# Performance work log

Hardware: AMD Instinct MI355X
Metric: run time of the kernel (lower is better)

The kernel has to match this reference:

```python
import jax, jax.numpy as jnp
import numpy as np

D_MODEL = 1024
D_STATE = 16
D_CONV = 4
EXPAND = 1
D_INNER = EXPAND * D_MODEL  # must equal D_MODEL for original dt_proj shapes to work
BATCH = 2
SEQ = 2048


def silu(x):
    return x * jax.nn.sigmoid(x)


def setup_inputs() -> dict:
    key = jax.random.key(0)
    ks = jax.random.split(key, 8)
    s = 0.02
    return {
        "x": jax.random.normal(ks[0], (BATCH, SEQ, D_MODEL), dtype=jnp.float32),
        "W_in": jax.random.normal(ks[1], (2 * D_INNER, D_MODEL), dtype=jnp.float32) * s,
        "conv_w": jax.random.normal(ks[2], (D_INNER, D_CONV), dtype=jnp.float32) * s,
        "conv_b": jnp.zeros((D_INNER,), dtype=jnp.float32),
        "W_dt": jax.random.normal(ks[3], (D_INNER, D_INNER), dtype=jnp.float32) * s,
        "b_dt": jnp.zeros((D_INNER,), dtype=jnp.float32),
        "A_log": jnp.zeros((D_INNER, D_STATE), dtype=jnp.float32),  # torch: log(ones)=0
        "Bp": jax.random.normal(ks[4], (D_INNER, D_STATE), dtype=jnp.float32),
        "Cp": jax.random.normal(ks[5], (D_INNER, D_STATE), dtype=jnp.float32),
        "Dp": jnp.ones((D_INNER,), dtype=jnp.float32),
        "W_out": jax.random.normal(ks[6], (D_MODEL, D_INNER), dtype=jnp.float32) * s,
    }


def reference(x, W_in, conv_w, conv_b, W_dt, b_dt, A_log, Bp, Cp, Dp, W_out):
    B, L, _ = x.shape
    # in_proj then split into ssm branch and gating residual
    xr = x @ W_in.T                               # (B, L, 2*D_INNER)
    x_proj, res = jnp.split(xr, 2, axis=-1)       # each (B, L, D_INNER)

    # causal depthwise conv1d (kernel D_CONV), == torch conv1d(padding=K-1)[..., :L]
    xp = jnp.pad(x_proj, ((0, 0), (D_CONV - 1, 0), (0, 0)))
    xc = conv_b + sum(conv_w[:, k] * xp[:, k:k + L, :] for k in range(D_CONV))
    xc = silu(xc)                                 # (B, L, D_INNER)

    # selective SSM scan
    delta = jax.nn.softplus(xc @ W_dt.T + b_dt)   # (B, L, D_INNER)
    A = -jnp.exp(A_log)                           # (D_INNER, D_STATE)
    dA = jnp.exp(delta[..., None] * A)            # (B, L, D_INNER, D_STATE)
    dBx = delta[..., None] * Bp * xc[..., None]   # (B, L, D_INNER, D_STATE)

    def step(h, inp):
        dA_t, dBx_t = inp                         # (B, D_INNER, D_STATE)
        h = dA_t * h + dBx_t
        y = jnp.einsum('bdn,dn->bd', h, Cp)
        return h, y

    h0 = jnp.zeros((B, D_INNER, D_STATE), dtype=x.dtype)
    _, ys = jax.lax.scan(step, h0, (dA.transpose(1, 0, 2, 3), dBx.transpose(1, 0, 2, 3)))
    x_ssm = ys.transpose(1, 0, 2) + xc * Dp       # (B, L, D_INNER)

    return (x_ssm * silu(res)) @ W_out.T          # (B, L, D_MODEL)
```

## Files before the change

### kernel.cpp

```cpp
#include <hip/hip_runtime.h>

typedef unsigned short u16;
typedef __bf16 bf16;
typedef bf16 bf16x8 __attribute__((ext_vector_type(8)));
typedef float f32x4 __attribute__((ext_vector_type(4)));

#define SEQ     2048
#define BATCH   2
#define DM      1024
#define DI      1024
#define NROW    (BATCH*SEQ)
#define NSTATE  16
#define NCHUNK  64
#define CLEN    32

static_assert(SEQ == NCHUNK * CLEN, "chunking must cover SEQ");

__device__ __forceinline__ u16 f2bf(float f) {
  unsigned u = __builtin_bit_cast(unsigned, f);
  u += 0x7FFFu + ((u >> 16) & 1u);
  return (u16)(u >> 16);
}
__device__ __forceinline__ float bf2f(u16 u) {
  return __builtin_bit_cast(float, (unsigned)u << 16);
}
__device__ __forceinline__ float sigm(float x) { return 1.f / (1.f + __expf(-x)); }

__global__ __launch_bounds__(256) void k_cvt_all(
    const float* __restrict__ x, const float* __restrict__ Win,
    const float* __restrict__ Wdt, const float* __restrict__ Wout,
    u16* __restrict__ xbf, u16* __restrict__ winbf,
    u16* __restrict__ wdtbf, u16* __restrict__ woutbf)
{
  long i = (long)blockIdx.x * 256 + threadIdx.x;
  const float* src; u16* dst; long off;
  if (i < 1048576)            { src = x;    dst = xbf;    off = i; }
  else if (i < 1572864)       { src = Win;  dst = winbf;  off = i - 1048576; }
  else if (i < 1835008)       { src = Wdt;  dst = wdtbf;  off = i - 1572864; }
  else                        { src = Wout; dst = woutbf; off = i - 1835008; }
  float4 v = reinterpret_cast<const float4*>(src)[off];
  ushort4 o;
  o.x = f2bf(v.x); o.y = f2bf(v.y); o.z = f2bf(v.z); o.w = f2bf(v.w);
  reinterpret_cast<ushort4*>(dst)[off] = o;
}


__device__ __forceinline__ void gload16(const u16* g, u16* l) {
  __builtin_amdgcn_global_load_lds((const __attribute__((address_space(1))) void*)g,
                                   (__attribute__((address_space(3))) void*)l,
                                   16, 0, 0);
}

template<int EPI, int GX>
__global__ __launch_bounds__(256, 2) void k_gemm(
    const u16* __restrict__ A, const u16* __restrict__ B,
    float* __restrict__ outf, u16* __restrict__ outb, u16* __restrict__ outb2,
    const float* __restrict__ bias,
    const float* __restrict__ A_log, const float* __restrict__ Bp,
    float* __restrict__ hfin, float* __restrict__ sumdt,
    int M, int N, int K)
{
  __shared__ __align__(16) u16 smem[4 * 128 * 64];
  u16* sA = smem;
  u16* sB = smem + 2 * 128 * 64;
  const int t = threadIdx.x;
  const int wave = t >> 6, lane = t & 63;
  const int lr = lane & 15, kb = lane >> 4;
  const int wr = wave >> 1, wc = wave & 1;

  const int nwg = gridDim.x, bid = blockIdx.x;
  const int wg  = (bid & 7) * (nwg >> 3) + (bid >> 3);
  const long bm = (long)(wg / GX) * 128;
  const long bn = (long)(wg % GX) * 128;

  f32x4 acc[4][4] = {};

  const int srow = t >> 3;
  const int gslot8 = (((t & 7) ^ (srow & 7)) * 8);
  const u16* gA0 = A + (bm + srow) * (long)K + gslot8;
  const u16* gB0 = B + (bn + srow) * (long)K + gslot8;

  auto STAGE = [&](int buf, int k0) {
    #pragma unroll
    for (int i = 0; i < 4; ++i)
      gload16(gA0 + (long)i * 32 * K + k0, &sA[buf * 8192 + i * 2048 + wave * 512]);
    #pragma unroll
    for (int i = 0; i < 4; ++i)
      gload16(gB0 + (long)i * 32 * K + k0, &sB[buf * 8192 + i * 2048 + wave * 512]);
  };

  const int xr = lr & 7;
  STAGE(0, 0);
  __syncthreads();
  int cur = 0;
  for (int k0 = 0; k0 < K; k0 += 64) {
    if (k0 + 64 < K) STAGE(cur ^ 1, k0 + 64);
    const u16* pa = &sA[cur * 8192];
    const u16* pb = &sB[cur * 8192];
    bf16x8 af[2][4], bfr[2][4];
    #pragma unroll
    for (int ks = 0; ks < 2; ++ks) {
      const int co = ((ks * 4 + kb) ^ xr) * 8;
      #pragma unroll
      for (int mi = 0; mi < 4; ++mi)
        af[ks][mi] = *reinterpret_cast<const bf16x8*>(
            pa + (wr * 64 + mi * 16 + lr) * 64 + co);
      #pragma unroll
      for (int ni = 0; ni < 4; ++ni)
        bfr[ks][ni] = *reinterpret_cast<const bf16x8*>(
            pb + (wc * 64 + ni * 16 + lr) * 64 + co);
    }
    __builtin_amdgcn_s_setprio(1);
    #pragma unroll
    for (int ks = 0; ks < 2; ++ks)
      #pragma unroll
      for (int mi = 0; mi < 4; ++mi)
        #pragma unroll
        for (int ni = 0; ni < 4; ++ni)
          acc[mi][ni] = __builtin_amdgcn_mfma_f32_16x16x32_bf16(
              af[ks][mi], bfr[ks][ni], acc[mi][ni], 0, 0, 0);
    __builtin_amdgcn_s_setprio(0);
    __syncthreads();
    cur ^= 1;
  }

  float* sDelta = (float*)smem;

  #pragma unroll
  for (int mi = 0; mi < 4; ++mi) {
    const long row0 = bm + wr * 64 + mi * 16 + kb * 4;
    #pragma unroll
    for (int ni = 0; ni < 4; ++ni) {
      const long col = bn + wc * 64 + ni * 16 + lr;
      #pragma unroll
      for (int j = 0; j < 4; ++j) {
        const float v = acc[mi][ni][j];
        const long r = row0 + j;
        if (EPI == 0) {
          outf[r * N + col] = v;
        } else if (EPI == 1) {
          if (bn < DI) outb[r * DI + col] = f2bf(v);
          else         outb2[r * DI + (col - DI)] = f2bf(v * sigm(v));
        } else if (EPI == 3) {
          float z = v + bias[col];
          float sp = fmaxf(z, 0.f) + log1pf(__expf(-fabsf(z)));
          outb[r * N + col] = f2bf(sp);
          sDelta[(int)(r - bm) * 128 + (int)(col - bn)] = sp;
        }
      }
    }
  }

  if (EPI == 3) {
    __syncthreads();
    const int dl = t & 127;
    const int d  = (int)bn + dl;
    const int b  = (int)(bm >> 11);
    const int c0 = (int)((bm & 2047) >> 5);
    float Aa[NSTATE], Bb[NSTATE];
    #pragma unroll
    for (int n = 0; n < NSTATE; ++n) {
      Aa[n] = -__expf(A_log[d * NSTATE + n]);
      Bb[n] = Bp[d * NSTATE + n];
    }
    for (int cl = (t >> 7) * 2; cl < (t >> 7) * 2 + 2; ++cl) {
      float h[NSTATE];
      #pragma unroll
      for (int n = 0; n < NSTATE; ++n) h[n] = 0.f;
      float sdt = 0.f;
      const long grow0 = bm + cl * 32;
      for (int i = 0; i < CLEN; ++i) {
        float dt = sDelta[(cl * 32 + i) * 128 + dl];
        float xv = bf2f(A[(grow0 + i) * (long)K + d]);
        sdt += dt;
        float dx = dt * xv;
        #pragma unroll
        for (int n = 0; n < NSTATE; ++n) {
          float da = __expf(dt * Aa[n]);
          h[n] = fmaf(da, h[n], dx * Bb[n]);
        }
      }
      const int cg = c0 + cl;
      const long hb = ((long)(b * NCHUNK + cg) * NSTATE) * DI + d;
      #pragma unroll
      for (int n = 0; n < NSTATE; ++n) hfin[hb + (long)n * DI] = h[n];
      sumdt[(long)(b * NCHUNK + cg) * DI + d] = sdt;
    }
  }
}

__global__ __launch_bounds__(256) void k_conv(
    const u16* __restrict__ xproj, const float* __restrict__ convw,
    const float* __restrict__ convb, u16* __restrict__ xcbf)
{
  const int idx = blockIdx.x * 256 + threadIdx.x;
  const int d0 = (idx & 127) * 8;
  const int m  = idx >> 7;
  const int l  = m & (SEQ - 1);
  float acc[8];
  #pragma unroll
  for (int di = 0; di < 8; ++di) acc[di] = convb[d0 + di];
  #pragma unroll
  for (int k = 0; k < 4; ++k) {
    if (l + k - 3 >= 0) {
      ushort4 v2 = *reinterpret_cast<const ushort4*>(&xproj[(long)(m + k - 3) * DI + d0]);
      ushort4 v3 = *reinterpret_cast<const ushort4*>(&xproj[(long)(m + k - 3) * DI + d0 + 4]);
      const u16 vv[8] = {v2.x, v2.y, v2.z, v2.w, v3.x, v3.y, v3.z, v3.w};
      #pragma unroll
      for (int di = 0; di < 8; ++di)
        acc[di] = fmaf(convw[(d0 + di) * 4 + k], bf2f(vv[di]), acc[di]);
    }
  }
  u16 ov[8];
  #pragma unroll
  for (int di = 0; di < 8; ++di) {
    float s = acc[di] * sigm(acc[di]);
    ov[di] = f2bf(s);
  }
  ushort4 o0 = {ov[0], ov[1], ov[2], ov[3]}, o1 = {ov[4], ov[5], ov[6], ov[7]};
  *reinterpret_cast<ushort4*>(&xcbf[(long)m * DI + d0]) = o0;
  *reinterpret_cast<ushort4*>(&xcbf[(long)m * DI + d0 + 4]) = o1;
}

__global__ __launch_bounds__(256) void k_combine(
    const float* __restrict__ hfin, const float* __restrict__ sumdt_buf,
    const float* __restrict__ A_log, float* __restrict__ hstart)
{
  const int idx = blockIdx.x * 256 + threadIdx.x;
  const int d = idx & (DI - 1);
  const int n = (idx >> 10) & (NSTATE - 1);
  const int b = idx >> 14;
  const float Aa = -__expf(A_log[d * NSTATE + n]);
  float h = 0.f;
  for (int c = 0; c < NCHUNK; ++c) {
    const long sb = ((long)(b * NCHUNK + c) * NSTATE + n) * DI + d;
    hstart[sb] = h;
    float sdt = sumdt_buf[(long)(b * NCHUNK + c) * DI + d];
    h = fmaf(__expf(Aa * sdt), h, hfin[sb]);
  }
}

__global__ __launch_bounds__(256) void k_scanB(
    const u16* __restrict__ delta, const u16* __restrict__ xc,
    const float* __restrict__ A_log, const float* __restrict__ Bp,
    const float* __restrict__ Cp, const float* __restrict__ Dp,
    const u16* __restrict__ sres, const float* __restrict__ hstart,
    u16* __restrict__ gated)
{
  const int tid = threadIdx.x, blk = blockIdx.x;
  const int d = (blk & 3) * 256 + tid;
  const int c = (blk >> 2) & (NCHUNK - 1);
  const int b = blk >> 8;
  float Aa[NSTATE], Bb[NSTATE], Cc[NSTATE], h[NSTATE];
  #pragma unroll
  for (int n = 0; n < NSTATE; ++n) {
    Aa[n] = -__expf(A_log[d * NSTATE + n]);
    Bb[n] = Bp[d * NSTATE + n];
    Cc[n] = Cp[d * NSTATE + n];
  }
  const float Dd = Dp[d];
  const long sb = ((long)(b * NCHUNK + c) * NSTATE) * DI + d;
  #pragma unroll
  for (int n = 0; n < NSTATE; ++n) h[n] = hstart[sb + (long)n * DI];
  const long base = ((long)(b * SEQ + c * CLEN)) * DI + d;
  for (int i = 0; i < CLEN; ++i) {
    float dt = bf2f(delta[base + (long)i * DI]);
    float x  = bf2f(xc[base + (long)i * DI]);
    float dx = dt * x;
    float y = 0.f;
    #pragma unroll
    for (int n = 0; n < NSTATE; ++n) {
      float da = __expf(dt * Aa[n]);
      h[n] = fmaf(da, h[n], dx * Bb[n]);
      y = fmaf(h[n], Cc[n], y);
    }
    float xs = fmaf(x, Dd, y);
    float g = xs * bf2f(sres[base + (long)i * DI]);
    gated[base + (long)i * DI] = f2bf(g);
  }
}

extern "C" void kernel_launch(void* const* d_in, const int* in_sizes, int n_in,
                              void* d_out, int out_size, void* d_ws, size_t ws_size,
                              hipStream_t stream)
{
  const float* x      = (const float*)d_in[0];
  const float* W_in   = (const float*)d_in[1];
  const float* conv_w = (const float*)d_in[2];
  const float* conv_b = (const float*)d_in[3];
  const float* W_dt   = (const float*)d_in[4];
  const float* b_dt   = (const float*)d_in[5];
  const float* A_log  = (const float*)d_in[6];
  const float* Bp     = (const float*)d_in[7];
  const float* Cp     = (const float*)d_in[8];
  const float* Dp     = (const float*)d_in[9];
  const float* W_out  = (const float*)d_in[10];
  float* out = (float*)d_out;

  const long MD = (long)NROW * DI;

  char* ws = (char*)d_ws;
  u16*   xproj_bf = (u16*)ws;               ws += MD * 2;
  u16*   silu_bf  = (u16*)ws;               ws += MD * 2;
  u16*   delta_bf = (u16*)ws;               ws += MD * 2;
  u16*   xc_bf    = (u16*)ws;               ws += MD * 2;
  u16*   xbf      = (u16*)ws;               ws += MD * 2;
  u16*   Win_bf   = (u16*)ws;               ws += (long)2 * DI * DM * 2;
  u16*   Wdt_bf   = (u16*)ws;               ws += (long)DI * DI * 2;
  u16*   Wout_bf  = (u16*)ws;               ws += (long)DM * DI * 2;
  float* hfin     = (float*)ws;             ws += (long)BATCH * NCHUNK * NSTATE * DI * 4;
  float* sumdt    = (float*)ws;             ws += (long)BATCH * NCHUNK * DI * 4;
  float* hstart   = (float*)ws;             ws += (long)BATCH * NCHUNK * NSTATE * DI * 4;

  u16* gated = xbf;

  k_cvt_all<<<dim3(8192), dim3(256), 0, stream>>>(
      x, W_in, W_dt, W_out, xbf, Win_bf, Wdt_bf, Wout_bf);

  k_gemm<1, 16><<<dim3(512), dim3(256), 0, stream>>>(
      xbf, Win_bf, nullptr, xproj_bf, silu_bf, nullptr,
      nullptr, nullptr, nullptr, nullptr, NROW, 2 * DI, DM);

  k_conv<<<dim3((unsigned)(MD / 8 / 256)), dim3(256), 0, stream>>>(
      xproj_bf, conv_w, conv_b, xc_bf);

  k_gemm<3, 8><<<dim3(256), dim3(256), 0, stream>>>(
      xc_bf, Wdt_bf, nullptr, delta_bf, nullptr, b_dt,
      A_log, Bp, hfin, sumdt, NROW, DI, DI);

  k_combine<<<dim3(BATCH * NSTATE * DI / 256), dim3(256), 0, stream>>>(
      hfin, sumdt, A_log, hstart);
  k_scanB<<<dim3(BATCH * NCHUNK * (DI / 256)), dim3(256), 0, stream>>>(
      delta_bf, xc_bf, A_log, Bp, Cp, Dp, silu_bf, hstart, gated);

  k_gemm<0, 8><<<dim3(256), dim3(256), 0, stream>>>(
      gated, Wout_bf, out, nullptr, nullptr, nullptr,
      nullptr, nullptr, nullptr, nullptr, NROW, DM, DI);
}
```

Measured before the change: 169.5 us.

## Switch GEMM main loop to a 4-stage LDS ring with K-tile 32

```diff
diff --git a/kernel.cpp b/kernel.cpp
--- a/kernel.cpp
+++ b/kernel.cpp
@@ -60,9 +60,9 @@
     float* __restrict__ hfin, float* __restrict__ sumdt,
     int M, int N, int K)
 {
-  __shared__ __align__(16) u16 smem[4 * 128 * 64];
+  __shared__ __align__(16) u16 smem[32768];
   u16* sA = smem;
-  u16* sB = smem + 2 * 128 * 64;
+  u16* sB = smem + 16384;
   const int t = threadIdx.x;
   const int wave = t >> 6, lane = t & 63;
   const int lr = lane & 15, kb = lane >> 4;
@@ -75,54 +75,44 @@
 
   f32x4 acc[4][4] = {};
 
-  const int srow = t >> 3;
-  const int gslot8 = (((t & 7) ^ (srow & 7)) * 8);
+  const int srow = t >> 2;
+  const int gslot8 = (((t & 3) ^ (srow & 3)) * 8);
   const u16* gA0 = A + (bm + srow) * (long)K + gslot8;
   const u16* gB0 = B + (bn + srow) * (long)K + gslot8;
 
   auto STAGE = [&](int buf, int k0) {
-    #pragma unroll
-    for (int i = 0; i < 4; ++i)
-      gload16(gA0 + (long)i * 32 * K + k0, &sA[buf * 8192 + i * 2048 + wave * 512]);
-    #pragma unroll
-    for (int i = 0; i < 4; ++i)
-      gload16(gB0 + (long)i * 32 * K + k0, &sB[buf * 8192 + i * 2048 + wave * 512]);
+    gload16(gA0 + k0,            &sA[buf * 4096 + wave * 512]);
+    gload16(gA0 + 64 * (long)K + k0, &sA[buf * 4096 + 2048 + wave * 512]);
+    gload16(gB0 + k0,            &sB[buf * 4096 + wave * 512]);
+    gload16(gB0 + 64 * (long)K + k0, &sB[buf * 4096 + 2048 + wave * 512]);
   };
 
-  const int xr = lr & 7;
+  const int xr = lr & 3;
+  const int NT = K / 32;
   STAGE(0, 0);
+  STAGE(1, 32);
+  for (int tt = 0; tt < NT; ++tt) {
+    STAGE((tt + 2) & 3, (tt + 2 < NT) ? (tt + 2) * 32 : 0);
+    asm volatile("s_waitcnt vmcnt(8)\n\ts_barrier" ::: "memory");
+    const int cur = tt & 3;
+    const u16* pa = &sA[cur * 4096];
+    const u16* pb = &sB[cur * 4096];
+    const int co = (kb ^ xr) * 8;
+    bf16x8 af[4], bfr[4];
+    #pragma unroll
+    for (int mi = 0; mi < 4; ++mi)
+      af[mi] = *reinterpret_cast<const bf16x8*>(pa + (wr * 64 + mi * 16 + lr) * 32 + co);
+    #pragma unroll
+    for (int ni = 0; ni < 4; ++ni)
+      bfr[ni] = *reinterpret_cast<const bf16x8*>(pb + (wc * 64 + ni * 16 + lr) * 32 + co);
+    #pragma unroll
+    for (int mi = 0; mi < 4; ++mi)
+      #pragma unroll
+      for (int ni = 0; ni < 4; ++ni)
+        acc[mi][ni] = __builtin_amdgcn_mfma_f32_16x16x32_bf16(
+            af[mi], bfr[ni], acc[mi][ni], 0, 0, 0);
+  }
   __syncthreads();
-  int cur = 0;
-  for (int k0 = 0; k0 < K; k0 += 64) {
-    if (k0 + 64 < K) STAGE(cur ^ 1, k0 + 64);
-    const u16* pa = &sA[cur * 8192];
-    const u16* pb = &sB[cur * 8192];
-    bf16x8 af[2][4], bfr[2][4];
-    #pragma unroll
-    for (int ks = 0; ks < 2; ++ks) {
-      const int co = ((ks * 4 + kb) ^ xr) * 8;
-      #pragma unroll
-      for (int mi = 0; mi < 4; ++mi)
-        af[ks][mi] = *reinterpret_cast<const bf16x8*>(
-            pa + (wr * 64 + mi * 16 + lr) * 64 + co);
-      #pragma unroll
-      for (int ni = 0; ni < 4; ++ni)
-        bfr[ks][ni] = *reinterpret_cast<const bf16x8*>(
-            pb + (wc * 64 + ni * 16 + lr) * 64 + co);
-    }
-    __builtin_amdgcn_s_setprio(1);
-    #pragma unroll
-    for (int ks = 0; ks < 2; ++ks)
-      #pragma unroll
-      for (int mi = 0; mi < 4; ++mi)
-        #pragma unroll
-        for (int ni = 0; ni < 4; ++ni)
-          acc[mi][ni] = __builtin_amdgcn_mfma_f32_16x16x32_bf16(
-              af[ks][mi], bfr[ks][ni], acc[mi][ni], 0, 0, 0);
-    __builtin_amdgcn_s_setprio(0);
-    __syncthreads();
-    cur ^= 1;
-  }
 
   float* sDelta = (float*)smem;
 
```

After: 172.3 us. No clear change (+1.7%).

## Split-K the two 1024-wide GEMMs and move scan prologue into reduction kernel

Applied to the files above, without the earlier changes.

```diff
diff --git a/kernel.cpp b/kernel.cpp
--- a/kernel.cpp
+++ b/kernel.cpp
@@ -4,6 +4,7 @@
 typedef __bf16 bf16;
 typedef bf16 bf16x8 __attribute__((ext_vector_type(8)));
 typedef float f32x4 __attribute__((ext_vector_type(4)));
+typedef float f32x16 __attribute__((ext_vector_type(16)));
 
 #define SEQ     2048
 #define BATCH   2
@@ -25,6 +26,12 @@
   return __builtin_bit_cast(float, (unsigned)u << 16);
 }
 __device__ __forceinline__ float sigm(float x) { return 1.f / (1.f + __expf(-x)); }
+
+__device__ __forceinline__ void gload16(const u16* g, u16* l) {
+  __builtin_amdgcn_global_load_lds((const __attribute__((address_space(1))) void*)g,
+                                   (__attribute__((address_space(3))) void*)l,
+                                   16, 0, 0);
+}
 
 __global__ __launch_bounds__(256) void k_cvt_all(
     const float* __restrict__ x, const float* __restrict__ Win,
@@ -44,36 +51,23 @@
   reinterpret_cast<ushort4*>(dst)[off] = o;
 }
 
-
-__device__ __forceinline__ void gload16(const u16* g, u16* l) {
-  __builtin_amdgcn_global_load_lds((const __attribute__((address_space(1))) void*)g,
-                                   (__attribute__((address_space(3))) void*)l,
-                                   16, 0, 0);
-}
-
-template<int EPI, int GX>
-__global__ __launch_bounds__(256, 2) void k_gemm(
+__global__ __launch_bounds__(256, 2) void k_gemm1(
     const u16* __restrict__ A, const u16* __restrict__ B,
-    float* __restrict__ outf, u16* __restrict__ outb, u16* __restrict__ outb2,
-    const float* __restrict__ bias,
-    const float* __restrict__ A_log, const float* __restrict__ Bp,
-    float* __restrict__ hfin, float* __restrict__ sumdt,
-    int M, int N, int K)
-{
-  __shared__ __align__(16) u16 smem[4 * 128 * 64];
-  u16* sA = smem;
-  u16* sB = smem + 2 * 128 * 64;
+    u16* __restrict__ outb, u16* __restrict__ outb2, int M, int N, int K)
+{
+  __shared__ __align__(16) u16 sA[2 * 128 * 64];
+  __shared__ __align__(16) u16 sB[2 * 128 * 64];
   const int t = threadIdx.x;
   const int wave = t >> 6, lane = t & 63;
-  const int lr = lane & 15, kb = lane >> 4;
+  const int la = lane & 31, hi = lane >> 5;
   const int wr = wave >> 1, wc = wave & 1;
 
   const int nwg = gridDim.x, bid = blockIdx.x;
   const int wg  = (bid & 7) * (nwg >> 3) + (bid >> 3);
-  const long bm = (long)(wg / GX) * 128;
-  const long bn = (long)(wg % GX) * 128;
-
-  f32x4 acc[4][4] = {};
+  const long bm = (long)(wg / 16) * 128;
+  const long bn = (long)(wg % 16) * 128;
+
+  f32x16 acc[2][2] = {};
 
   const int srow = t >> 3;
   const int gslot8 = (((t & 7) ^ (srow & 7)) * 8);
@@ -89,7 +83,7 @@
       gload16(gB0 + (long)i * 32 * K + k0, &sB[buf * 8192 + i * 2048 + wave * 512]);
   };
 
-  const int xr = lr & 7;
+  const int xr = la & 7;
   STAGE(0, 0);
   __syncthreads();
   int cur = 0;
@@ -97,35 +91,109 @@
     if (k0 + 64 < K) STAGE(cur ^ 1, k0 + 64);
     const u16* pa = &sA[cur * 8192];
     const u16* pb = &sB[cur * 8192];
-    bf16x8 af[2][4], bfr[2][4];
-    #pragma unroll
-    for (int ks = 0; ks < 2; ++ks) {
-      const int co = ((ks * 4 + kb) ^ xr) * 8;
-      #pragma unroll
-      for (int mi = 0; mi < 4; ++mi)
-        af[ks][mi] = *reinterpret_cast<const bf16x8*>(
-            pa + (wr * 64 + mi * 16 + lr) * 64 + co);
-      #pragma unroll
-      for (int ni = 0; ni < 4; ++ni)
-        bfr[ks][ni] = *reinterpret_cast<const bf16x8*>(
-            pb + (wc * 64 + ni * 16 + lr) * 64 + co);
-    }
-    __builtin_amdgcn_s_setprio(1);
-    #pragma unroll
-    for (int ks = 0; ks < 2; ++ks)
-      #pragma unroll
-      for (int mi = 0; mi < 4; ++mi)
+    bf16x8 af[4][2], bfr[4][2];
+    #pragma unroll
+    for (int ks = 0; ks < 4; ++ks) {
+      const int co = ((ks * 2 + hi) ^ xr) * 8;
+      #pragma unroll
+      for (int mi = 0; mi < 2; ++mi)
+        af[ks][mi] = *reinterpret_cast<const bf16x8*>(pa + (wr * 64 + mi * 32 + la) * 64 + co);
+      #pragma unroll
+      for (int ni = 0; ni < 2; ++ni)
+        bfr[ks][ni] = *reinterpret_cast<const bf16x8*>(pb + (wc * 64 + ni * 32 + la) * 64 + co);
+    }
+    #pragma unroll
+    for (int ks = 0; ks < 4; ++ks)
+      #pragma unroll
+      for (int mi = 0; mi < 2; ++mi)
         #pragma unroll
-        for (int ni = 0; ni < 4; ++ni)
-          acc[mi][ni] = __builtin_amdgcn_mfma_f32_16x16x32_bf16(
+        for (int ni = 0; ni < 2; ++ni)
+          acc[mi][ni] = __builtin_amdgcn_mfma_f32_32x32x16_bf16(
               af[ks][mi], bfr[ks][ni], acc[mi][ni], 0, 0, 0);
-    __builtin_amdgcn_s_setprio(0);
     __syncthreads();
     cur ^= 1;
   }
 
-  float* sDelta = (float*)smem;
-
+  #pragma unroll
+  for (int mi = 0; mi < 2; ++mi) {
+    const long rowb = bm + wr * 64 + mi * 32 + 4 * hi;
+    #pragma unroll
+    for (int ni = 0; ni < 2; ++ni) {
+      const long col = bn + wc * 64 + ni * 32 + la;
+      #pragma unroll
+      for (int q = 0; q < 4; ++q)
+        #pragma unroll
+        for (int j = 0; j < 4; ++j) {
+          const float v = acc[mi][ni][q * 4 + j];
+          const long r = rowb + q * 8 + j;
+          if (bn < DI) outb[r * DI + col] = f2bf(v);
+          else         outb2[r * DI + (col - DI)] = f2bf(v * sigm(v));
+        }
+    }
+  }
+}
+
+__global__ __launch_bounds__(256, 2) void k_gemm_sk(
+    const u16* __restrict__ A, const u16* __restrict__ B,
+    float* __restrict__ part, int M, int N, int K)
+{
+  __shared__ __align__(16) u16 sA[2 * 128 * 32];
+  __shared__ __align__(16) u16 sB[2 * 128 * 32];
+  const int t = threadIdx.x;
+  const int wave = t >> 6, lane = t & 63;
+  const int lr = lane & 15, kb = lane >> 4;
+  const int wr = wave >> 1, wc = wave & 1;
+
+  const int nwg = gridDim.x, bid = blockIdx.x;
+  const int wg  = (bid & 7) * (nwg >> 3) + (bid >> 3);
+  const int ks  = wg >> 8;
+  const int rem = wg & 255;
+  const long bm = (long)(rem >> 3) * 128;
+  const long bn = (long)(rem & 7) * 128;
+  const int kbase = ks * (K / 2);
+
+  f32x4 acc[4][4] = {};
+
+  const int srow = t >> 2;
+  const int gslot8 = (((t & 3) ^ (srow & 3)) * 8);
+  const u16* gA0 = A + (bm + srow) * (long)K + gslot8 + kbase;
+  const u16* gB0 = B + (bn + srow) * (long)K + gslot8 + kbase;
+
+  auto STAGE = [&](int buf, int k0) {
+    gload16(gA0 + k0,                &sA[buf * 4096 + wave * 512]);
+    gload16(gA0 + 64 * (long)K + k0, &sA[buf * 4096 + 2048 + wave * 512]);
+    gload16(gB0 + k0,                &sB[buf * 4096 + wave * 512]);
+    gload16(gB0 + 64 * (long)K + k0, &sB[buf * 4096 + 2048 + wave * 512]);
+  };
+
+  const int xr = lr & 3;
+  const int co = ((kb ^ xr) * 8);
+  STAGE(0, 0);
+  __syncthreads();
+  int cur = 0;
+  const int KS = K / 2;
+  for (int k0 = 0; k0 < KS; k0 += 32) {
+    if (k0 + 32 < KS) STAGE(cur ^ 1, k0 + 32);
+    const u16* pa = &sA[cur * 4096];
+    const u16* pb = &sB[cur * 4096];
+    bf16x8 af[4], bfr[4];
+    #pragma unroll
+    for (int mi = 0; mi < 4; ++mi)
+      af[mi] = *reinterpret_cast<const bf16x8*>(pa + (wr * 64 + mi * 16 + lr) * 32 + co);
+    #pragma unroll
+    for (int ni = 0; ni < 4; ++ni)
+      bfr[ni] = *reinterpret_cast<const bf16x8*>(pb + (wc * 64 + ni * 16 + lr) * 32 + co);
+    #pragma unroll
+    for (int mi = 0; mi < 4; ++mi)
+      #pragma unroll
+      for (int ni = 0; ni < 4; ++ni)
+        acc[mi][ni] = __builtin_amdgcn_mfma_f32_16x16x32_bf16(
+            af[mi], bfr[ni], acc[mi][ni], 0, 0, 0);
+    __syncthreads();
+    cur ^= 1;
+  }
+
+  float* po = part + (long)ks * M * N;
   #pragma unroll
   for (int mi = 0; mi < 4; ++mi) {
     const long row0 = bm + wr * 64 + mi * 16 + kb * 4;
@@ -133,60 +201,85 @@
     for (int ni = 0; ni < 4; ++ni) {
       const long col = bn + wc * 64 + ni * 16 + lr;
       #pragma unroll
-      for (int j = 0; j < 4; ++j) {
-        const float v = acc[mi][ni][j];
-        const long r = row0 + j;
-        if (EPI == 0) {
-          outf[r * N + col] = v;
-        } else if (EPI == 1) {
-          if (bn < DI) outb[r * DI + col] = f2bf(v);
-          else         outb2[r * DI + (col - DI)] = f2bf(v * sigm(v));
-        } else if (EPI == 3) {
-          float z = v + bias[col];
-          float sp = fmaxf(z, 0.f) + log1pf(__expf(-fabsf(z)));
-          outb[r * N + col] = f2bf(sp);
-          sDelta[(int)(r - bm) * 128 + (int)(col - bn)] = sp;
-        }
-      }
-    }
-  }
-
-  if (EPI == 3) {
-    __syncthreads();
-    const int dl = t & 127;
-    const int d  = (int)bn + dl;
-    const int b  = (int)(bm >> 11);
-    const int c0 = (int)((bm & 2047) >> 5);
-    float Aa[NSTATE], Bb[NSTATE];
-    #pragma unroll
-    for (int n = 0; n < NSTATE; ++n) {
-      Aa[n] = -__expf(A_log[d * NSTATE + n]);
-      Bb[n] = Bp[d * NSTATE + n];
-    }
-    for (int cl = (t >> 7) * 2; cl < (t >> 7) * 2 + 2; ++cl) {
-      float h[NSTATE];
-      #pragma unroll
-      for (int n = 0; n < NSTATE; ++n) h[n] = 0.f;
-      float sdt = 0.f;
-      const long grow0 = bm + cl * 32;
-      for (int i = 0; i < CLEN; ++i) {
-        float dt = sDelta[(cl * 32 + i) * 128 + dl];
-        float xv = bf2f(A[(grow0 + i) * (long)K + d]);
-        sdt += dt;
-        float dx = dt * xv;
-        #pragma unroll
-        for (int n = 0; n < NSTATE; ++n) {
-          float da = __expf(dt * Aa[n]);
-          h[n] = fmaf(da, h[n], dx * Bb[n]);
-        }
-      }
-      const int cg = c0 + cl;
-      const long hb = ((long)(b * NCHUNK + cg) * NSTATE) * DI + d;
-      #pragma unroll
-      for (int n = 0; n < NSTATE; ++n) hfin[hb + (long)n * DI] = h[n];
-      sumdt[(long)(b * NCHUNK + cg) * DI + d] = sdt;
-    }
-  }
+      for (int j = 0; j < 4; ++j)
+        po[(row0 + j) * N + col] = acc[mi][ni][j];
+    }
+  }
+}
+
+__global__ __launch_bounds__(256) void k_redG2(
+    const float* __restrict__ part, const float* __restrict__ bias,
+    const u16* __restrict__ xc, const float* __restrict__ A_log,
+    const float* __restrict__ Bp, u16* __restrict__ delta_bf,
+    float* __restrict__ hfin, float* __restrict__ sumdt)
+{
+  __shared__ float sD[32 * 128];
+  const int t = threadIdx.x;
+  const int c  = blockIdx.x >> 3;
+  const int db = blockIdx.x & 7;
+  const int r0 = c * 32;
+  const int d0 = db * 128;
+  const float* p0 = part;
+  const float* p1 = part + (long)NROW * DI;
+
+  #pragma unroll
+  for (int v = 0; v < 4; ++v) {
+    const int e = t + v * 256;
+    const int row = e >> 5, cf = (e & 31) * 4;
+    const long gi = (long)(r0 + row) * DI + d0 + cf;
+    float4 a = *reinterpret_cast<const float4*>(&p0[gi]);
+    float4 b = *reinterpret_cast<const float4*>(&p1[gi]);
+    float z0 = a.x + b.x + bias[d0 + cf + 0];
+    float z1 = a.y + b.y + bias[d0 + cf + 1];
+    float z2 = a.z + b.z + bias[d0 + cf + 2];
+    float z3 = a.w + b.w + bias[d0 + cf + 3];
+    float s0 = fmaxf(z0, 0.f) + log1pf(__expf(-fabsf(z0)));
+    float s1 = fmaxf(z1, 0.f) + log1pf(__expf(-fabsf(z1)));
+    float s2 = fmaxf(z2, 0.f) + log1pf(__expf(-fabsf(z2)));
+    float s3 = fmaxf(z3, 0.f) + log1pf(__expf(-fabsf(z3)));
+    ushort4 o = {f2bf(s0), f2bf(s1), f2bf(s2), f2bf(s3)};
+    *reinterpret_cast<ushort4*>(&delta_bf[gi]) = o;
+    sD[row * 128 + cf] = s0; sD[row * 128 + cf + 1] = s1;
+    sD[row * 128 + cf + 2] = s2; sD[row * 128 + cf + 3] = s3;
+  }
+  __syncthreads();
+
+  const int dl = t & 127, half = t >> 7;
+  const int d = d0 + dl;
+  const int b = c >> 6, cb = c & 63;
+  float Aa[8], Bb[8], h[8];
+  #pragma unroll
+  for (int n = 0; n < 8; ++n) {
+    Aa[n] = -__expf(A_log[d * NSTATE + half * 8 + n]);
+    Bb[n] = Bp[d * NSTATE + half * 8 + n];
+    h[n] = 0.f;
+  }
+  float sdt = 0.f;
+  for (int i = 0; i < CLEN; ++i) {
+    float dt = sD[i * 128 + dl];
+    float xv = bf2f(xc[(long)(r0 + i) * DI + d]);
+    sdt += dt;
+    float dx = dt * xv;
+    #pragma unroll
+    for (int n = 0; n < 8; ++n) {
+      float da = __expf(dt * Aa[n]);
+      h[n] = fmaf(da, h[n], dx * Bb[n]);
+    }
+  }
+  const long hb = ((long)(b * NCHUNK + cb) * NSTATE + half * 8) * DI + d;
+  #pragma unroll
+  for (int n = 0; n < 8; ++n) hfin[hb + (long)n * DI] = h[n];
+  if (half == 0) sumdt[(long)(b * NCHUNK + cb) * DI + d] = sdt;
+}
+
+__global__ __launch_bounds__(256) void k_redG3(
+    const float* __restrict__ part, float* __restrict__ out)
+{
+  const long i = (long)blockIdx.x * 256 + threadIdx.x;
+  const float4 a = reinterpret_cast<const float4*>(part)[i];
+  const float4 b = reinterpret_cast<const float4*>(part + (long)NROW * DM)[i];
+  float4 o = {a.x + b.x, a.y + b.y, a.z + b.z, a.w + b.w};
+  reinterpret_cast<float4*>(out)[i] = o;
 }
 
 __global__ __launch_bounds__(256) void k_conv(
@@ -311,29 +404,30 @@
   float* hfin     = (float*)ws;             ws += (long)BATCH * NCHUNK * NSTATE * DI * 4;
   float* sumdt    = (float*)ws;             ws += (long)BATCH * NCHUNK * DI * 4;
   float* hstart   = (float*)ws;             ws += (long)BATCH * NCHUNK * NSTATE * DI * 4;
+  float* part     = (float*)ws;             ws += MD * 2 * 4;
 
   u16* gated = xbf;
 
   k_cvt_all<<<dim3(8192), dim3(256), 0, stream>>>(
       x, W_in, W_dt, W_out, xbf, Win_bf, Wdt_bf, Wout_bf);
 
-  k_gemm<1, 16><<<dim3(512), dim3(256), 0, stream>>>(
-      xbf, Win_bf, nullptr, xproj_bf, silu_bf, nullptr,
-      nullptr, nullptr, nullptr, nullptr, NROW, 2 * DI, DM);
+  k_gemm1<<<dim3(512), dim3(256), 0, stream>>>(
+      xbf, Win_bf, xproj_bf, silu_bf, NROW, 2 * DI, DM);
 
   k_conv<<<dim3((unsigned)(MD / 8 / 256)), dim3(256), 0, stream>>>(
       xproj_bf, conv_w, conv_b, xc_bf);
 
-  k_gemm<3, 8><<<dim3(256), dim3(256), 0, stream>>>(
-      xc_bf, Wdt_bf, nullptr, delta_bf, nullptr, b_dt,
-      A_log, Bp, hfin, sumdt, NROW, DI, DI);
+  k_gemm_sk<<<dim3(512), dim3(256), 0, stream>>>(
+      xc_bf, Wdt_bf, part, NROW, DI, DI);
+  k_redG2<<<dim3(1024), dim3(256), 0, stream>>>(
+      part, b_dt, xc_bf, A_log, Bp, delta_bf, hfin, sumdt);
 
   k_combine<<<dim3(BATCH * NSTATE * DI / 256), dim3(256), 0, stream>>>(
       hfin, sumdt, A_log, hstart);
   k_scanB<<<dim3(BATCH * NCHUNK * (DI / 256)), dim3(256), 0, stream>>>(
       delta_bf, xc_bf, A_log, Bp, Cp, Dp, silu_bf, hstart, gated);
 
-  k_gemm<0, 8><<<dim3(256), dim3(256), 0, stream>>>(
-      gated, Wout_bf, out, nullptr, nullptr, nullptr,
-      nullptr, nullptr, nullptr, nullptr, NROW, DM, DI);
-}
+  k_gemm_sk<<<dim3(512), dim3(256), 0, stream>>>(
+      gated, Wout_bf, part, NROW, DM, DI);
+  k_redG3<<<dim3((unsigned)(MD / 4 / 256)), dim3(256), 0, stream>>>(part, out);
+}
```

After: 177.3 us. +4.6%, slower.

## Split-K within block for 256-tile GEMMs and use 32x32 MFMA for in_proj

Applied to the files above, without the earlier changes.

```diff
diff --git a/kernel.cpp b/kernel.cpp
--- a/kernel.cpp
+++ b/kernel.cpp
@@ -4,6 +4,7 @@
 typedef __bf16 bf16;
 typedef bf16 bf16x8 __attribute__((ext_vector_type(8)));
 typedef float f32x4 __attribute__((ext_vector_type(4)));
+typedef float f32x16 __attribute__((ext_vector_type(16)));
 
 #define SEQ     2048
 #define BATCH   2
@@ -25,6 +26,12 @@
   return __builtin_bit_cast(float, (unsigned)u << 16);
 }
 __device__ __forceinline__ float sigm(float x) { return 1.f / (1.f + __expf(-x)); }
+
+__device__ __forceinline__ void gload16(const u16* g, u16* l) {
+  __builtin_amdgcn_global_load_lds((const __attribute__((address_space(1))) void*)g,
+                                   (__attribute__((address_space(3))) void*)l,
+                                   16, 0, 0);
+}
 
 __global__ __launch_bounds__(256) void k_cvt_all(
     const float* __restrict__ x, const float* __restrict__ Win,
@@ -44,36 +51,23 @@
   reinterpret_cast<ushort4*>(dst)[off] = o;
 }
 
-
-__device__ __forceinline__ void gload16(const u16* g, u16* l) {
-  __builtin_amdgcn_global_load_lds((const __attribute__((address_space(1))) void*)g,
-                                   (__attribute__((address_space(3))) void*)l,
-                                   16, 0, 0);
-}
-
-template<int EPI, int GX>
-__global__ __launch_bounds__(256, 2) void k_gemm(
+__global__ __launch_bounds__(256, 2) void k_gemm1(
     const u16* __restrict__ A, const u16* __restrict__ B,
-    float* __restrict__ outf, u16* __restrict__ outb, u16* __restrict__ outb2,
-    const float* __restrict__ bias,
-    const float* __restrict__ A_log, const float* __restrict__ Bp,
-    float* __restrict__ hfin, float* __restrict__ sumdt,
-    int M, int N, int K)
-{
-  __shared__ __align__(16) u16 smem[4 * 128 * 64];
-  u16* sA = smem;
-  u16* sB = smem + 2 * 128 * 64;
+    u16* __restrict__ outb, u16* __restrict__ outb2, int M, int N, int K)
+{
+  __shared__ __align__(16) u16 sA[2 * 128 * 64];
+  __shared__ __align__(16) u16 sB[2 * 128 * 64];
   const int t = threadIdx.x;
   const int wave = t >> 6, lane = t & 63;
-  const int lr = lane & 15, kb = lane >> 4;
+  const int la = lane & 31, hi = lane >> 5;
   const int wr = wave >> 1, wc = wave & 1;
 
   const int nwg = gridDim.x, bid = blockIdx.x;
   const int wg  = (bid & 7) * (nwg >> 3) + (bid >> 3);
-  const long bm = (long)(wg / GX) * 128;
-  const long bn = (long)(wg % GX) * 128;
-
-  f32x4 acc[4][4] = {};
+  const long bm = (long)(wg / 16) * 128;
+  const long bn = (long)(wg % 16) * 128;
+
+  f32x16 acc[2][2] = {};
 
   const int srow = t >> 3;
   const int gslot8 = (((t & 7) ^ (srow & 7)) * 8);
@@ -89,7 +83,7 @@
       gload16(gB0 + (long)i * 32 * K + k0, &sB[buf * 8192 + i * 2048 + wave * 512]);
   };
 
-  const int xr = lr & 7;
+  const int xr = la & 7;
   STAGE(0, 0);
   __syncthreads();
   int cur = 0;
@@ -97,55 +91,155 @@
     if (k0 + 64 < K) STAGE(cur ^ 1, k0 + 64);
     const u16* pa = &sA[cur * 8192];
     const u16* pb = &sB[cur * 8192];
-    bf16x8 af[2][4], bfr[2][4];
-    #pragma unroll
-    for (int ks = 0; ks < 2; ++ks) {
-      const int co = ((ks * 4 + kb) ^ xr) * 8;
-      #pragma unroll
-      for (int mi = 0; mi < 4; ++mi)
-        af[ks][mi] = *reinterpret_cast<const bf16x8*>(
-            pa + (wr * 64 + mi * 16 + lr) * 64 + co);
-      #pragma unroll
-      for (int ni = 0; ni < 4; ++ni)
-        bfr[ks][ni] = *reinterpret_cast<const bf16x8*>(
-            pb + (wc * 64 + ni * 16 + lr) * 64 + co);
-    }
-    __builtin_amdgcn_s_setprio(1);
-    #pragma unroll
-    for (int ks = 0; ks < 2; ++ks)
-      #pragma unroll
-      for (int mi = 0; mi < 4; ++mi)
+    bf16x8 af[4][2], bfr[4][2];
+    #pragma unroll
+    for (int ks = 0; ks < 4; ++ks) {
+      const int co = ((ks * 2 + hi) ^ xr) * 8;
+      #pragma unroll
+      for (int mi = 0; mi < 2; ++mi)
+        af[ks][mi] = *reinterpret_cast<const bf16x8*>(pa + (wr * 64 + mi * 32 + la) * 64 + co);
+      #pragma unroll
+      for (int ni = 0; ni < 2; ++ni)
+        bfr[ks][ni] = *reinterpret_cast<const bf16x8*>(pb + (wc * 64 + ni * 32 + la) * 64 + co);
+    }
+    #pragma unroll
+    for (int ks = 0; ks < 4; ++ks)
+      #pragma unroll
+      for (int mi = 0; mi < 2; ++mi)
         #pragma unroll
-        for (int ni = 0; ni < 4; ++ni)
-          acc[mi][ni] = __builtin_amdgcn_mfma_f32_16x16x32_bf16(
+        for (int ni = 0; ni < 2; ++ni)
+          acc[mi][ni] = __builtin_amdgcn_mfma_f32_32x32x16_bf16(
               af[ks][mi], bfr[ks][ni], acc[mi][ni], 0, 0, 0);
-    __builtin_amdgcn_s_setprio(0);
     __syncthreads();
     cur ^= 1;
   }
 
-  float* sDelta = (float*)smem;
-
-  #pragma unroll
-  for (int mi = 0; mi < 4; ++mi) {
-    const long row0 = bm + wr * 64 + mi * 16 + kb * 4;
-    #pragma unroll
-    for (int ni = 0; ni < 4; ++ni) {
-      const long col = bn + wc * 64 + ni * 16 + lr;
-      #pragma unroll
-      for (int j = 0; j < 4; ++j) {
-        const float v = acc[mi][ni][j];
-        const long r = row0 + j;
-        if (EPI == 0) {
-          outf[r * N + col] = v;
-        } else if (EPI == 1) {
+  #pragma unroll
+  for (int mi = 0; mi < 2; ++mi) {
+    const long rowb = bm + wr * 64 + mi * 32 + 4 * hi;
+    #pragma unroll
+    for (int ni = 0; ni < 2; ++ni) {
+      const long col = bn + wc * 64 + ni * 32 + la;
+      #pragma unroll
+      for (int q = 0; q < 4; ++q)
+        #pragma unroll
+        for (int j = 0; j < 4; ++j) {
+          const float v = acc[mi][ni][q * 4 + j];
+          const long r = rowb + q * 8 + j;
           if (bn < DI) outb[r * DI + col] = f2bf(v);
           else         outb2[r * DI + (col - DI)] = f2bf(v * sigm(v));
-        } else if (EPI == 3) {
-          float z = v + bias[col];
-          float sp = fmaxf(z, 0.f) + log1pf(__expf(-fabsf(z)));
-          outb[r * N + col] = f2bf(sp);
-          sDelta[(int)(r - bm) * 128 + (int)(col - bn)] = sp;
+        }
+    }
+  }
+}
+
+template<int EPI>
+__global__ __launch_bounds__(512, 1) void k_gemm_skb(
+    const u16* __restrict__ A, const u16* __restrict__ B,
+    float* __restrict__ outf, u16* __restrict__ outb,
+    const float* __restrict__ bias,
+    const float* __restrict__ A_log, const float* __restrict__ Bp,
+    float* __restrict__ hfin, float* __restrict__ sumdt,
+    int M, int N, int K)
+{
+  __shared__ __align__(16) u16 sStage[32768];
+  __shared__ __align__(16) float sX[16384];
+  const int t = threadIdx.x;
+  const int g  = t >> 8;
+  const int tg = t & 255;
+  const int wl = (t >> 6) & 3;
+  const int lane = t & 63;
+  const int lr = lane & 15, kb = lane >> 4;
+  const int wr = wl >> 1, wc = wl & 1;
+
+  const int bid = blockIdx.x;
+  const int wg  = (bid & 7) * 32 + (bid >> 3);
+  const long bm = (long)(wg >> 3) * 128;
+  const long bn = (long)(wg & 7) * 128;
+  const int kbase = g * (K / 2);
+
+  f32x4 acc[4][4] = {};
+
+  const int srow = tg >> 2;
+  const int gslot8 = (((tg & 3) ^ (srow & 3)) * 8);
+  const u16* gA0 = A + (bm + srow) * (long)K + gslot8 + kbase;
+  const u16* gB0 = B + (bn + srow) * (long)K + gslot8 + kbase;
+  u16* lbase = &sStage[g * 16384];
+  const int wig = wl * 512;
+
+  auto STAGE = [&](int buf, int k0) {
+    gload16(gA0 + k0,                 lbase + buf * 8192 + wig);
+    gload16(gA0 + 64 * (long)K + k0,  lbase + buf * 8192 + 2048 + wig);
+    gload16(gB0 + k0,                 lbase + buf * 8192 + 4096 + wig);
+    gload16(gB0 + 64 * (long)K + k0,  lbase + buf * 8192 + 6144 + wig);
+  };
+
+  const int co = ((kb ^ (lr & 3)) * 8);
+  STAGE(0, 0);
+  __syncthreads();
+  int cur = 0;
+  const int KS = K / 2;
+  for (int k0 = 0; k0 < KS; k0 += 32) {
+    if (k0 + 32 < KS) STAGE(cur ^ 1, k0 + 32);
+    const u16* pa = lbase + cur * 8192;
+    const u16* pb = pa + 4096;
+    bf16x8 af[4], bfr[4];
+    #pragma unroll
+    for (int mi = 0; mi < 4; ++mi)
+      af[mi] = *reinterpret_cast<const bf16x8*>(pa + (wr * 64 + mi * 16 + lr) * 32 + co);
+    #pragma unroll
+    for (int ni = 0; ni < 4; ++ni)
+      bfr[ni] = *reinterpret_cast<const bf16x8*>(pb + (wc * 64 + ni * 16 + lr) * 32 + co);
+    #pragma unroll
+    for (int mi = 0; mi < 4; ++mi)
+      #pragma unroll
+      for (int ni = 0; ni < 4; ++ni)
+        acc[mi][ni] = __builtin_amdgcn_mfma_f32_16x16x32_bf16(
+            af[mi], bfr[ni], acc[mi][ni], 0, 0, 0);
+    __syncthreads();
+    cur ^= 1;
+  }
+
+  if (g == 1) {
+    #pragma unroll
+    for (int mi = 0; mi < 4; ++mi)
+      #pragma unroll
+      for (int ni = 0; ni < 4; ++ni)
+        #pragma unroll
+        for (int j = 0; j < 4; ++j)
+          sX[(mi * 16 + ni * 4 + j) * 256 + tg] = acc[mi][ni][j];
+  }
+  __syncthreads();
+  if (g == 0) {
+    #pragma unroll
+    for (int mi = 0; mi < 4; ++mi)
+      #pragma unroll
+      for (int ni = 0; ni < 4; ++ni)
+        #pragma unroll
+        for (int j = 0; j < 4; ++j)
+          acc[mi][ni][j] += sX[(mi * 16 + ni * 4 + j) * 256 + tg];
+  }
+  if (EPI == 3) __syncthreads();
+
+  if (g == 0) {
+    #pragma unroll
+    for (int mi = 0; mi < 4; ++mi) {
+      const long row0 = bm + wr * 64 + mi * 16 + kb * 4;
+      #pragma unroll
+      for (int ni = 0; ni < 4; ++ni) {
+        const long col = bn + wc * 64 + ni * 16 + lr;
+        #pragma unroll
+        for (int j = 0; j < 4; ++j) {
+          const float v = acc[mi][ni][j];
+          const long r = row0 + j;
+          if (EPI == 0) {
+            outf[r * N + col] = v;
+          } else {
+            float z = v + bias[col];
+            float sp = fmaxf(z, 0.f) + log1pf(__expf(-fabsf(z)));
+            outb[r * N + col] = f2bf(sp);
+            sX[(int)(r - bm) * 128 + (int)(col - bn)] = sp;
+          }
         }
       }
     }
@@ -154,38 +248,34 @@
   if (EPI == 3) {
     __syncthreads();
     const int dl = t & 127;
+    const int cl = t >> 7;
     const int d  = (int)bn + dl;
     const int b  = (int)(bm >> 11);
-    const int c0 = (int)((bm & 2047) >> 5);
-    float Aa[NSTATE], Bb[NSTATE];
+    const int cg = (int)((bm & 2047) >> 5) + cl;
+    float Aa[NSTATE], Bb[NSTATE], h[NSTATE];
     #pragma unroll
     for (int n = 0; n < NSTATE; ++n) {
       Aa[n] = -__expf(A_log[d * NSTATE + n]);
       Bb[n] = Bp[d * NSTATE + n];
-    }
-    for (int cl = (t >> 7) * 2; cl < (t >> 7) * 2 + 2; ++cl) {
-      float h[NSTATE];
-      #pragma unroll
-      for (int n = 0; n < NSTATE; ++n) h[n] = 0.f;
-      float sdt = 0.f;
-      const long grow0 = bm + cl * 32;
-      for (int i = 0; i < CLEN; ++i) {
-        float dt = sDelta[(cl * 32 + i) * 128 + dl];
-        float xv = bf2f(A[(grow0 + i) * (long)K + d]);
-        sdt += dt;
-        float dx = dt * xv;
-        #pragma unroll
-        for (int n = 0; n < NSTATE; ++n) {
-          float da = __expf(dt * Aa[n]);
-          h[n] = fmaf(da, h[n], dx * Bb[n]);
-        }
+      h[n] = 0.f;
+    }
+    float sdt = 0.f;
+    const long grow0 = bm + cl * 32;
+    for (int i = 0; i < CLEN; ++i) {
+      float dt = sX[(cl * 32 + i) * 128 + dl];
+      float xv = bf2f(A[(grow0 + i) * (long)K + d]);
+      sdt += dt;
+      float dx = dt * xv;
+      #pragma unroll
+      for (int n = 0; n < NSTATE; ++n) {
+        float da = __expf(dt * Aa[n]);
+        h[n] = fmaf(da, h[n], dx * Bb[n]);
       }
-      const int cg = c0 + cl;
-      const long hb = ((long)(b * NCHUNK + cg) * NSTATE) * DI + d;
-      #pragma unroll
-      for (int n = 0; n < NSTATE; ++n) hfin[hb + (long)n * DI] = h[n];
-      sumdt[(long)(b * NCHUNK + cg) * DI + d] = sdt;
-    }
+    }
+    const long hb = ((long)(b * NCHUNK + cg) * NSTATE) * DI + d;
+    #pragma unroll
+    for (int n = 0; n < NSTATE; ++n) hfin[hb + (long)n * DI] = h[n];
+    sumdt[(long)(b * NCHUNK + cg) * DI + d] = sdt;
   }
 }
 
@@ -317,15 +407,14 @@
   k_cvt_all<<<dim3(8192), dim3(256), 0, stream>>>(
       x, W_in, W_dt, W_out, xbf, Win_bf, Wdt_bf, Wout_bf);
 
-  k_gemm<1, 16><<<dim3(512), dim3(256), 0, stream>>>(
-      xbf, Win_bf, nullptr, xproj_bf, silu_bf, nullptr,
-      nullptr, nullptr, nullptr, nullptr, NROW, 2 * DI, DM);
+  k_gemm1<<<dim3(512), dim3(256), 0, stream>>>(
+      xbf, Win_bf, xproj_bf, silu_bf, NROW, 2 * DI, DM);
 
   k_conv<<<dim3((unsigned)(MD / 8 / 256)), dim3(256), 0, stream>>>(
       xproj_bf, conv_w, conv_b, xc_bf);
 
-  k_gemm<3, 8><<<dim3(256), dim3(256), 0, stream>>>(
-      xc_bf, Wdt_bf, nullptr, delta_bf, nullptr, b_dt,
+  k_gemm_skb<3><<<dim3(256), dim3(512), 0, stream>>>(
+      xc_bf, Wdt_bf, nullptr, delta_bf, b_dt,
       A_log, Bp, hfin, sumdt, NROW, DI, DI);
 
   k_combine<<<dim3(BATCH * NSTATE * DI / 256), dim3(256), 0, stream>>>(
@@ -333,7 +422,7 @@
   k_scanB<<<dim3(BATCH * NCHUNK * (DI / 256)), dim3(256), 0, stream>>>(
       delta_bf, xc_bf, A_log, Bp, Cp, Dp, silu_bf, hstart, gated);
 
-  k_gemm<0, 8><<<dim3(256), dim3(256), 0, stream>>>(
-      gated, Wout_bf, out, nullptr, nullptr, nullptr,
+  k_gemm_skb<0><<<dim3(256), dim3(512), 0, stream>>>(
+      gated, Wout_bf, out, nullptr, nullptr,
       nullptr, nullptr, nullptr, nullptr, NROW, DM, DI);
 }
```

Measured after the change: 177.2 us. 1.05x slower.
